# Kernel optimization log

Measured on AMD Instinct MI355X. Metric: run time of the kernel, lower is better.

## Reference

```python
import jax, jax.numpy as jnp
import numpy as np

C = 256
C8 = C // 8


def setup_inputs() -> dict:
    key = jax.random.key(0)
    ks = jax.random.split(key, 9)
    B, H, W = 4, 64, 64
    s = 1.0 / np.sqrt(C)
    return {
        "pre_feat": jax.random.normal(ks[0], (B, C, H, W), jnp.float32),
        "post_feat": jax.random.normal(ks[1], (B, C, H, W), jnp.float32),
        "Wq": jax.random.normal(ks[2], (C8, C), jnp.float32) * s,
        "bq": jnp.zeros((C8,), jnp.float32),
        "Wk": jax.random.normal(ks[3], (C8, C), jnp.float32) * s,
        "bk": jnp.zeros((C8,), jnp.float32),
        "Wv": jax.random.normal(ks[4], (C, C), jnp.float32) * s,
        "bv": jnp.zeros((C,), jnp.float32),
        "gamma": jnp.zeros((1,), jnp.float32),
    }


def reference(pre_feat, post_feat, Wq, bq, Wk, bk, Wv, bv, gamma):
    B, Cc, H, W = pre_feat.shape
    N = H * W
    pre = pre_feat.reshape(B, Cc, N)    # (B, C, N)
    post = post_feat.reshape(B, Cc, N)
    # 1x1 convs == per-pixel linear projections
    q = jnp.einsum('dc,bcn->bdn', Wq, post) + bq[None, :, None]  # (B, C8, N)
    k = jnp.einsum('dc,bcn->bdn', Wk, pre) + bk[None, :, None]   # (B, C8, N)
    v = jnp.einsum('dc,bcn->bdn', Wv, pre) + bv[None, :, None]   # (B, C, N)
    # energy[b,i,j] = <q[b,:,i], k[b,:,j]>  (unscaled)
    energy = jnp.einsum('bdi,bdj->bij', q, k)                    # (B, N, N)
    attention = jax.nn.softmax(energy, axis=-1)
    # out[b,c,i] = sum_j v[b,c,j] * attention[b,i,j]
    out = jnp.einsum('bcj,bij->bci', v, attention).reshape(B, Cc, H, W)
    return gamma[0] * out + post_feat
```

## Files before the change

kernel.cpp:

```cpp
#include <hip/hip_runtime.h>
#include <hip/hip_bf16.h>

#define Bn 4
#define Cn 256
#define Dn 32
#define Nn 4096

typedef __bf16 bf16x8 __attribute__((ext_vector_type(8)));
typedef float f32x4 __attribute__((ext_vector_type(4)));

__device__ __forceinline__ float bf2f(unsigned short u) {
  unsigned int v = ((unsigned int)u) << 16;
  return __builtin_bit_cast(float, v);
}
__device__ __forceinline__ unsigned short f2bf(float f) {
  unsigned int v = __builtin_bit_cast(unsigned int, f);
  v += 0x7FFFu + ((v >> 16) & 1u);
  return (unsigned short)(v >> 16);
}
__device__ __forceinline__ unsigned int pk2(float a, float b) {
  union { __hip_bfloat162 h; unsigned int u; } x;
  x.h = __float22bfloat162_rn(make_float2(a, b));
  return x.u;
}
__device__ __forceinline__ bf16x8 ldfrag(const unsigned short* p) {
  return __builtin_bit_cast(bf16x8, *(const uint4*)p);
}
__device__ __forceinline__ uint4 pack8(const float* p) {
  float4 a = *(const float4*)p;
  float4 b = *(const float4*)(p + 4);
  union { unsigned int u2[4]; uint4 u; } x;
  x.u2[0] = pk2(a.x, a.y); x.u2[1] = pk2(a.z, a.w);
  x.u2[2] = pk2(b.x, b.y); x.u2[3] = pk2(b.z, b.w);
  return x.u;
}
__device__ __forceinline__ bf16x8 ldfrag_f32(const float* p) {
  float4 a = *(const float4*)p;
  float4 b = *(const float4*)(p + 4);
  union { unsigned int u2[4]; bf16x8 v; } x;
  x.u2[0] = pk2(a.x, a.y); x.u2[1] = pk2(a.z, a.w);
  x.u2[2] = pk2(b.x, b.y); x.u2[3] = pk2(b.z, b.w);
  return x.v;
}
__device__ __forceinline__ void async16(unsigned short* lds, const unsigned short* g) {
  __builtin_amdgcn_global_load_lds(
      (const __attribute__((address_space(1))) unsigned int*)g,
      (__attribute__((address_space(3))) unsigned int*)lds, 16, 0, 0);
}

__global__ __launch_bounds__(256) void qkprep(
    const float* __restrict__ pre, const float* __restrict__ post,
    const float* __restrict__ Wq, const float* __restrict__ bq,
    const float* __restrict__ Wk, const float* __restrict__ bk,
    const float* __restrict__ Wv,
    unsigned short* __restrict__ Qt, unsigned short* __restrict__ Kt,
    unsigned short* __restrict__ preBf, unsigned short* __restrict__ WvBf)
{
  const int blk = blockIdx.x, tid = threadIdx.x;
  if (blk >= 512) {
    if (blk < 1024) {
      size_t base = ((size_t)(blk - 512) * 256 + tid) * 32;
#pragma unroll
      for (int u = 0; u < 4; u++)
        *(uint4*)(preBf + base + u * 8) = pack8(pre + base + u * 8);
    } else {
      size_t base = ((size_t)(blk - 1024) * 256 + tid) * 32;
#pragma unroll
      for (int u = 0; u < 4; u++)
        *(uint4*)(WvBf + base + u * 8) = pack8(Wv + base + u * 8);
    }
    return;
  }
  const int lane = tid & 63, w = tid >> 6;
  const int quad = lane >> 4, n16 = lane & 15;
  const int b = blk >> 7;
  const int i0 = (blk & 127) << 5;
  const int isub = w & 1, dh = w >> 1;
  const int i = i0 + isub * 16 + n16;

  const f32x4 zz = {0.f, 0.f, 0.f, 0.f};
  f32x4 aq = zz, ak = zz;
  const float* postB = post + (size_t)b * Cn * Nn + i;
  const float* preB  = pre  + (size_t)b * Cn * Nn + i;

#pragma unroll
  for (int kc = 0; kc < 8; kc++) {
    const int c0 = kc * 32 + quad * 8;
    const float* pp = postB + (size_t)c0 * Nn;
    const float* pr = preB + (size_t)c0 * Nn;
    union { unsigned int u2[4]; bf16x8 v; } bp, bq8;
#pragma unroll
    for (int e2 = 0; e2 < 4; e2++) {
      float p0 = pp[(size_t)(2 * e2) * Nn], p1 = pp[(size_t)(2 * e2 + 1) * Nn];
      float r0 = pr[(size_t)(2 * e2) * Nn], r1 = pr[(size_t)(2 * e2 + 1) * Nn];
      bp.u2[e2] = pk2(p0, p1);
      bq8.u2[e2] = pk2(r0, r1);
    }
    bf16x8 awq = ldfrag_f32(Wq + (size_t)(dh * 16 + n16) * Cn + kc * 32 + quad * 8);
    bf16x8 awk = ldfrag_f32(Wk + (size_t)(dh * 16 + n16) * Cn + kc * 32 + quad * 8);
    aq = __builtin_amdgcn_mfma_f32_16x16x32_bf16(awq, bp.v, aq, 0, 0, 0);
    ak = __builtin_amdgcn_mfma_f32_16x16x32_bf16(awk, bq8.v, ak, 0, 0, 0);
  }
  const float LOG2E = 1.44269504f;
  union { unsigned short s[4]; uint2 u; } oq, ok;
#pragma unroll
  for (int r = 0; r < 4; r++) {
    int d = dh * 16 + quad * 4 + r;
    oq.s[r] = f2bf((aq[r] + bq[d]) * LOG2E);
    ok.s[r] = f2bf(ak[r] + bk[d]);
  }
  *(uint2*)(Qt + ((size_t)b * Nn + i) * Dn + dh * 16 + quad * 4) = oq.u;
  *(uint2*)(Kt + ((size_t)b * Nn + i) * Dn + dh * 16 + quad * 4) = ok.u;
}

__global__ __launch_bounds__(256) void flash_attn(
    const unsigned short* __restrict__ Qt, const unsigned short* __restrict__ Kt,
    const unsigned short* __restrict__ preBf,
    unsigned short* __restrict__ Opart, float* __restrict__ Lpart)
{
  __shared__ __align__(16) unsigned short sX[256 * 64];
  __shared__ __align__(16) unsigned short Pl[64 * 72];

  const int tid = threadIdx.x;
  const int lane = tid & 63, w = tid >> 6;
  const int quad = lane >> 4, n16 = lane & 15;
  const int b = blockIdx.x >> 8;
  const int js = (blockIdx.x >> 6) & 3;
  const int it = blockIdx.x & 63;
  const int i0 = it * 64;
  const int jbase = js * 1024;

  const bf16x8 qf = ldfrag(Qt + ((size_t)b * Nn + i0 + w * 16 + n16) * Dn + quad * 8);

  const f32x4 zz = {0.f, 0.f, 0.f, 0.f};
  f32x4 acc[4][4];
#pragma unroll
  for (int sub = 0; sub < 4; sub++)
#pragma unroll
    for (int ct = 0; ct < 4; ct++) acc[sub][ct] = zz;
  float lrow = 0.f;

  const size_t laneoff = (size_t)(lane >> 3) * Nn + (size_t)(((lane & 7) ^ (lane >> 3)) << 3);
  const unsigned short* preB = preBf + (size_t)b * Cn * Nn + laneoff;
  const int xsw = n16 & 7;
  const int xoff0 = (quad ^ xsw) << 3;
  const int xoff1 = ((4 + quad) ^ xsw) << 3;

  for (int t = 0; t < 16; ++t) {
    const int j0 = jbase + t * 64;
    __syncthreads();
#pragma unroll
    for (int k = 0; k < 8; k++) {
      const int rb = (k * 4 + w) * 8;
      async16(sX + rb * 64 + (lane << 3), preB + (size_t)rb * Nn + j0);
    }
    {
      f32x4 sc[4];
#pragma unroll
      for (int jt = 0; jt < 4; jt++) {
        bf16x8 akf = ldfrag(Kt + ((size_t)b * Nn + j0 + jt * 16 + n16) * Dn + quad * 8);
        sc[jt] = __builtin_amdgcn_mfma_f32_16x16x32_bf16(akf, qf, zz, 0, 0, 0);
      }
      float ps = 0.f;
#pragma unroll
      for (int jt = 0; jt < 4; jt++) {
        float p0 = exp2f(fminf(sc[jt][0], 101.f));
        float p1 = exp2f(fminf(sc[jt][1], 101.f));
        float p2 = exp2f(fminf(sc[jt][2], 101.f));
        float p3 = exp2f(fminf(sc[jt][3], 101.f));
        ps += (p0 + p1) + (p2 + p3);
        union { unsigned int u2[2]; uint2 u; } pk;
        pk.u2[0] = pk2(p0, p1);
        pk.u2[1] = pk2(p2, p3);
        *(uint2*)&Pl[(size_t)(w * 16 + n16) * 72 + jt * 16 + quad * 4] = pk.u;
      }
      ps += __shfl_xor(ps, 16);
      ps += __shfl_xor(ps, 32);
      lrow += ps;
    }
    __syncthreads();

#pragma unroll
    for (int kc = 0; kc < 2; kc++) {
      const int xo = kc ? xoff1 : xoff0;
      bf16x8 pB[4];
#pragma unroll
      for (int sub = 0; sub < 4; sub++)
        pB[sub] = ldfrag(&Pl[(size_t)(sub * 16 + n16) * 72 + kc * 32 + quad * 8]);
#pragma unroll
      for (int ct = 0; ct < 4; ct++) {
        const int crow = w * 64 + ct * 16 + n16;
        bf16x8 av = ldfrag(&sX[crow * 64 + xo]);
        acc[0][ct] = __builtin_amdgcn_mfma_f32_16x16x32_bf16(av, pB[0], acc[0][ct], 0, 0, 0);
        acc[1][ct] = __builtin_amdgcn_mfma_f32_16x16x32_bf16(av, pB[1], acc[1][ct], 0, 0, 0);
        acc[2][ct] = __builtin_amdgcn_mfma_f32_16x16x32_bf16(av, pB[2], acc[2][ct], 0, 0, 0);
        acc[3][ct] = __builtin_amdgcn_mfma_f32_16x16x32_bf16(av, pB[3], acc[3][ct], 0, 0, 0);
      }
    }
  }

  const size_t pbase = (size_t)(js * 4 + b) * Nn;
  if (quad == 0) Lpart[pbase + i0 + w * 16 + n16] = lrow;
#pragma unroll
  for (int sub = 0; sub < 4; sub++) {
    const int i = i0 + sub * 16 + n16;
#pragma unroll
    for (int ct = 0; ct < 4; ct++) {
      union { unsigned int u2[2]; uint2 u; } pk;
      pk.u2[0] = pk2(acc[sub][ct][0], acc[sub][ct][1]);
      pk.u2[1] = pk2(acc[sub][ct][2], acc[sub][ct][3]);
      *(uint2*)(Opart + (pbase + i) * 256 + w * 64 + ct * 16 + quad * 4) = pk.u;
    }
  }
}

__global__ __launch_bounds__(256) void combine(
    const unsigned short* __restrict__ Opart, const float* __restrict__ Lpart,
    const unsigned short* __restrict__ WvBf, const float* __restrict__ bv,
    const float* __restrict__ post, const float* __restrict__ gamma,
    float* __restrict__ out)
{
  __shared__ __align__(16) unsigned short sU[16 * 264];
  __shared__ float sL[16];

  const int tid = threadIdx.x;
  const int lane = tid & 63, w = tid >> 6;
  const int quad = lane >> 4, n16 = lane & 15;
  const int b = blockIdx.x >> 8;
  const int i0 = (blockIdx.x & 255) << 4;

  if (tid < 16) {
    float l = 0.f;
#pragma unroll
    for (int js = 0; js < 4; js++) l += Lpart[(size_t)(js * 4 + b) * Nn + i0 + tid];
    sL[tid] = 1.f / l;
  }
  __syncthreads();

#pragma unroll
  for (int pass = 0; pass < 2; pass++) {
    const int s = tid + pass * 256;
    const int il = s >> 5, c8 = (s & 31) << 3;
    const float inv = sL[il];
    float a[8] = {0.f, 0.f, 0.f, 0.f, 0.f, 0.f, 0.f, 0.f};
#pragma unroll
    for (int js = 0; js < 4; js++) {
      uint4 uu = *(const uint4*)(Opart + ((size_t)(js * 4 + b) * Nn + i0 + il) * 256 + c8);
      const unsigned short* us = (const unsigned short*)&uu;
#pragma unroll
      for (int e = 0; e < 8; e++) a[e] += bf2f(us[e]);
    }
    union { unsigned int u2[4]; uint4 u; } pk;
#pragma unroll
    for (int e2 = 0; e2 < 4; e2++) pk.u2[e2] = pk2(a[2 * e2] * inv, a[2 * e2 + 1] * inv);
    *(uint4*)&sU[il * 264 + c8] = pk.u;
  }
  __syncthreads();

  bf16x8 ub[8];
#pragma unroll
  for (int kc = 0; kc < 8; kc++)
    ub[kc] = ldfrag(&sU[n16 * 264 + kc * 32 + quad * 8]);

  const float g = gamma[0];
  const f32x4 zz = {0.f, 0.f, 0.f, 0.f};
#pragma unroll
  for (int e = 0; e < 4; e++) {
    const int ct2 = w * 4 + e;
    f32x4 o = zz;
#pragma unroll
    for (int kc = 0; kc < 8; kc++) {
      bf16x8 awv = ldfrag(WvBf + (size_t)(ct2 * 16 + n16) * Cn + kc * 32 + quad * 8);
      o = __builtin_amdgcn_mfma_f32_16x16x32_bf16(awv, ub[kc], o, 0, 0, 0);
    }
#pragma unroll
    for (int r = 0; r < 4; r++) {
      const int c = ct2 * 16 + quad * 4 + r;
      const size_t addr = ((size_t)b * Cn + c) * Nn + i0 + n16;
      out[addr] = g * (o[r] + bv[c]) + post[addr];
    }
  }
}

extern "C" void kernel_launch(void* const* d_in, const int* in_sizes, int n_in,
                              void* d_out, int out_size, void* d_ws, size_t ws_size,
                              hipStream_t stream) {
  const float* pre   = (const float*)d_in[0];
  const float* post  = (const float*)d_in[1];
  const float* Wq    = (const float*)d_in[2];
  const float* bq    = (const float*)d_in[3];
  const float* Wk    = (const float*)d_in[4];
  const float* bk    = (const float*)d_in[5];
  const float* Wv    = (const float*)d_in[6];
  const float* bv    = (const float*)d_in[7];
  const float* gamma = (const float*)d_in[8];
  float* out = (float*)d_out;

  unsigned short* ws = (unsigned short*)d_ws;
  unsigned short* Qt    = ws;
  unsigned short* Kt    = Qt + (size_t)Bn * Nn * Dn;
  unsigned short* preBf = Kt + (size_t)Bn * Nn * Dn;
  unsigned short* WvBf  = preBf + (size_t)Bn * Cn * Nn;
  float* Lpart = (float*)(WvBf + Cn * Cn);
  unsigned short* Opart = (unsigned short*)(Lpart + 4 * Bn * Nn);

  qkprep<<<1032, 256, 0, stream>>>(pre, post, Wq, bq, Wk, bk, Wv,
                                   Qt, Kt, preBf, WvBf);
  flash_attn<<<1024, 256, 0, stream>>>(Qt, Kt, preBf, Opart, Lpart);
  combine<<<1024, 256, 0, stream>>>(Opart, Lpart, WvBf, bv, post, gamma, out);
}
```

Before: 202.7 us.

## Load value fragments directly from global, drop LDS staging, double-buffer P

The flash_attn kernel no longer stages the bf16 pre-feature tile in shared memory through async global-to-LDS loads. Each wave now reads its MFMA A-fragments straight from global memory, which cuts LDS from about 41KB to about 18KB. A double-buffered P tile lets one barrier per iteration go away, and the launch bounds now ask for 4 blocks per CU. The catch is uncoalesced 16-byte global reads per lane that rely on L2/L1 caching, with no prefetch overlap.

```diff
diff --git a/kernel.cpp b/kernel.cpp
--- a/kernel.cpp
+++ b/kernel.cpp
@@ -41,11 +41,6 @@
   x.u2[0] = pk2(a.x, a.y); x.u2[1] = pk2(a.z, a.w);
   x.u2[2] = pk2(b.x, b.y); x.u2[3] = pk2(b.z, b.w);
   return x.v;
-}
-__device__ __forceinline__ void async16(unsigned short* lds, const unsigned short* g) {
-  __builtin_amdgcn_global_load_lds(
-      (const __attribute__((address_space(1))) unsigned int*)g,
-      (__attribute__((address_space(3))) unsigned int*)lds, 16, 0, 0);
 }
 
 __global__ __launch_bounds__(256) void qkprep(
@@ -113,13 +108,12 @@
   *(uint2*)(Kt + ((size_t)b * Nn + i) * Dn + dh * 16 + quad * 4) = ok.u;
 }
 
-__global__ __launch_bounds__(256) void flash_attn(
+__global__ __launch_bounds__(256, 4) void flash_attn(
     const unsigned short* __restrict__ Qt, const unsigned short* __restrict__ Kt,
     const unsigned short* __restrict__ preBf,
     unsigned short* __restrict__ Opart, float* __restrict__ Lpart)
 {
-  __shared__ __align__(16) unsigned short sX[256 * 64];
-  __shared__ __align__(16) unsigned short Pl[64 * 72];
+  __shared__ __align__(16) unsigned short Pl[2][64 * 72];
 
   const int tid = threadIdx.x;
   const int lane = tid & 63, w = tid >> 6;
@@ -140,25 +134,18 @@
     for (int ct = 0; ct < 4; ct++) acc[sub][ct] = zz;
   float lrow = 0.f;
 
-  const size_t laneoff = (size_t)(lane >> 3) * Nn + (size_t)(((lane & 7) ^ (lane >> 3)) << 3);
-  const unsigned short* preB = preBf + (size_t)b * Cn * Nn + laneoff;
-  const int xsw = n16 & 7;
-  const int xoff0 = (quad ^ xsw) << 3;
-  const int xoff1 = ((4 + quad) ^ xsw) << 3;
+  const unsigned short* pK = Kt + ((size_t)b * Nn + n16) * Dn + quad * 8;
+  const unsigned short* pX = preBf + ((size_t)b * Cn + w * 64 + n16) * Nn + quad * 8;
 
   for (int t = 0; t < 16; ++t) {
     const int j0 = jbase + t * 64;
-    __syncthreads();
-#pragma unroll
-    for (int k = 0; k < 8; k++) {
-      const int rb = (k * 4 + w) * 8;
-      async16(sX + rb * 64 + (lane << 3), preB + (size_t)rb * Nn + j0);
-    }
+    const int buf = t & 1;
+
     {
       f32x4 sc[4];
 #pragma unroll
       for (int jt = 0; jt < 4; jt++) {
-        bf16x8 akf = ldfrag(Kt + ((size_t)b * Nn + j0 + jt * 16 + n16) * Dn + quad * 8);
+        bf16x8 akf = ldfrag(pK + (size_t)(j0 + jt * 16) * Dn);
         sc[jt] = __builtin_amdgcn_mfma_f32_16x16x32_bf16(akf, qf, zz, 0, 0, 0);
       }
       float ps = 0.f;
@@ -172,7 +159,7 @@
         union { unsigned int u2[2]; uint2 u; } pk;
         pk.u2[0] = pk2(p0, p1);
         pk.u2[1] = pk2(p2, p3);
-        *(uint2*)&Pl[(size_t)(w * 16 + n16) * 72 + jt * 16 + quad * 4] = pk.u;
+        *(uint2*)&Pl[buf][(size_t)(w * 16 + n16) * 72 + jt * 16 + quad * 4] = pk.u;
       }
       ps += __shfl_xor(ps, 16);
       ps += __shfl_xor(ps, 32);
@@ -182,15 +169,13 @@
 
 #pragma unroll
     for (int kc = 0; kc < 2; kc++) {
-      const int xo = kc ? xoff1 : xoff0;
       bf16x8 pB[4];
 #pragma unroll
       for (int sub = 0; sub < 4; sub++)
-        pB[sub] = ldfrag(&Pl[(size_t)(sub * 16 + n16) * 72 + kc * 32 + quad * 8]);
+        pB[sub] = ldfrag(&Pl[buf][(size_t)(sub * 16 + n16) * 72 + kc * 32 + quad * 8]);
 #pragma unroll
       for (int ct = 0; ct < 4; ct++) {
-        const int crow = w * 64 + ct * 16 + n16;
-        bf16x8 av = ldfrag(&sX[crow * 64 + xo]);
+        bf16x8 av = ldfrag(pX + (size_t)(ct * 16) * Nn + j0 + kc * 32);
         acc[0][ct] = __builtin_amdgcn_mfma_f32_16x16x32_bf16(av, pB[0], acc[0][ct], 0, 0, 0);
         acc[1][ct] = __builtin_amdgcn_mfma_f32_16x16x32_bf16(av, pB[1], acc[1][ct], 0, 0, 0);
         acc[2][ct] = __builtin_amdgcn_mfma_f32_16x16x32_bf16(av, pB[2], acc[2][ct], 0, 0, 0);
```

Measured after the change: 221.9 us. +9.5%, slower.
